# Kernel optimization log

Measured on AMD Instinct MI355X. Metric: run time of the kernel, lower is better.

The kernel has to match this reference:

```python
import jax, jax.numpy as jnp
import numpy as np

B, L, D, H = 2, 1000, 288, 8
DIM = D // H          # 36 per-head dim
DFF = 2 * D           # 576 conv-FFN hidden
KS = L // 4           # 250 sampled keys per query
NQ = L // 4           # 250 selected (active) queries
EPS = 1e-5


def _layernorm(x, g, b):
    mu = x.mean(-1, keepdims=True)
    var = ((x - mu) ** 2).mean(-1, keepdims=True)
    return (x - mu) * jax.lax.rsqrt(var + EPS) * g + b


def _prob_attention(q, k, v, index_key):
    # q,k,v: [b,h,L,dim]; index_key: [L, KS]
    b, h, l, dim = q.shape
    # sample KS keys per query row (gather): [b,h,L,KS,dim]
    k_samp = jnp.take(k, index_key, axis=2)
    # sampled scores: [b,h,L,KS]
    scores_samp = jnp.einsum('bhld,bhlkd->bhlk', q, k_samp)
    # sparsity measure M(q) = max - mean(over full l_key, as in source)
    measure = scores_samp.max(-1) - scores_samp.sum(-1) / l
    # top-NQ active queries per (b,h): [b,h,NQ]
    idx_q = jax.lax.top_k(measure, NQ)[1]
    q_sel = jnp.take_along_axis(q, idx_q[..., None], axis=2)  # [b,h,NQ,dim]
    sim = jnp.einsum('bhqd,bhkd->bhqk', q_sel, k) * (1.0 / np.sqrt(dim))
    attn = jax.nn.softmax(sim, axis=-1)
    out_sel = jnp.einsum('bhqk,bhkd->bhqd', attn, v)          # [b,h,NQ,dim]
    # lazy queries get mean(V); scatter active outputs in
    out = jnp.broadcast_to(v.mean(axis=2, keepdims=True), v.shape)
    bi = jnp.arange(b)[:, None, None]
    hi = jnp.arange(h)[None, :, None]
    out = out.at[bi, hi, idx_q].set(out_sel)
    return out  # [b,h,L,dim]


def reference(x, index_key, Wq, bq, Wk, bk, Wv, bv, W1, b1, W2, b2,
              ln1_g, ln1_b, ln2_g, ln2_b):
    b, l, d = x.shape
    # QKV projections -> [b,h,L,dim]
    q = (x @ Wq.T + bq).reshape(b, l, H, DIM).transpose(0, 2, 1, 3)
    k = (x @ Wk.T + bk).reshape(b, l, H, DIM).transpose(0, 2, 1, 3)
    v = (x @ Wv.T + bv).reshape(b, l, H, DIM).transpose(0, 2, 1, 3)
    attn = _prob_attention(q, k, v, index_key)
    attn = attn.transpose(0, 2, 1, 3).reshape(b, l, d)
    # residual + LN1 (dropout is identity in eval)
    h1 = _layernorm(x + attn, ln1_g, ln1_b)
    # conv FFN (kernel_size=1 conv == per-position linear), exact GELU
    f = jax.nn.gelu(h1 @ W1.T + b1, approximate=False)   # [b,l,DFF]
    f = jax.nn.gelu(f @ W2.T + b2, approximate=False)    # [b,l,d]
    return _layernorm(f + h1, ln2_g, ln2_b)


def setup_inputs() -> dict:
    key = jax.random.key(0)
    ks = jax.random.split(key, 10)
    s = 0.05
    return {
        'x': jax.random.normal(ks[0], (B, L, D), jnp.float32),
        'index_key': jax.random.randint(ks[1], (L, KS), 0, L),
        'Wq': jax.random.normal(ks[2], (D, D), jnp.float32) * s,
        'bq': jnp.zeros((D,), jnp.float32),
        'Wk': jax.random.normal(ks[3], (D, D), jnp.float32) * s,
        'bk': jnp.zeros((D,), jnp.float32),
        'Wv': jax.random.normal(ks[4], (D, D), jnp.float32) * s,
        'bv': jnp.zeros((D,), jnp.float32),
        'W1': jax.random.normal(ks[5], (DFF, D), jnp.float32) * s,
        'b1': jnp.zeros((DFF,), jnp.float32),
        'W2': jax.random.normal(ks[6], (D, DFF), jnp.float32) * s,
        'b2': jnp.zeros((D,), jnp.float32),
        'ln1_g': jnp.ones((D,), jnp.float32),
        'ln1_b': jnp.zeros((D,), jnp.float32),
        'ln2_g': jnp.ones((D,), jnp.float32),
        'ln2_b': jnp.zeros((D,), jnp.float32),
    }
```

## Files before the change

### kernel.cpp

```cpp
#include <hip/hip_runtime.h>
#include <math.h>

#define B_ 2
#define L_ 1000
#define D_ 288
#define H_ 8
#define DIM_ 36
#define DFF_ 576
#define KS_ 250
#define NQ_ 250
#define BH_ (B_ * H_)
#define EPS_ 1e-5f
#define PSTRIDE_ 40
#define MAXCL_ 125

__device__ __forceinline__ float gelu_exact(float x) {
    return 0.5f * x * (1.0f + erff(x * 0.70710678118654752f));
}

__device__ __forceinline__ float dot4(float4 a, float4 b) {
    return a.x * b.x + a.y * b.y + a.z * b.z + a.w * b.w;
}

__global__ __launch_bounds__(256) void weights_prep_kernel(
    const float* __restrict__ Wq, const float* __restrict__ Wk,
    const float* __restrict__ Wv,
    float* __restrict__ WqT, float* __restrict__ WkT, float* __restrict__ WvT,
    const float* __restrict__ W1, const float* __restrict__ W2,
    float* __restrict__ W1T, float* __restrict__ W2T)
{
    __shared__ float tile[32][33];
    const int tx = threadIdx.x & 31, ty = threadIdx.x >> 5;
    if (blockIdx.x < 243) {
        const int m = blockIdx.x / 81;
        const int t = blockIdx.x % 81;
        const float* src = (m == 0) ? Wq : (m == 1) ? Wk : Wv;
        float* dst = (m == 0) ? WqT : (m == 1) ? WkT : WvT;
        const int ty0 = (t / 9) * 32, tx0 = (t % 9) * 32;
#pragma unroll
        for (int i = 0; i < 4; i++)
            tile[ty + 8 * i][tx] = src[(size_t)(ty0 + ty + 8 * i) * D_ + tx0 + tx];
        __syncthreads();
#pragma unroll
        for (int i = 0; i < 4; i++)
            dst[(size_t)(tx0 + ty + 8 * i) * D_ + ty0 + tx] = tile[tx][ty + 8 * i];
    } else {
        int t = blockIdx.x - 243;
        const float* src; float* dst; int Rr, Cc, ntx;
        if (t < 162) { src = W1; dst = W1T; Rr = DFF_; Cc = D_; ntx = 9; }
        else { t -= 162; src = W2; dst = W2T; Rr = D_; Cc = DFF_; ntx = 18; }
        const int ty0 = (t / ntx) * 32, tx0 = (t % ntx) * 32;
#pragma unroll
        for (int i = 0; i < 4; i++)
            tile[ty + 8 * i][tx] = src[(size_t)(ty0 + ty + 8 * i) * Cc + tx0 + tx];
        __syncthreads();
#pragma unroll
        for (int i = 0; i < 4; i++)
            dst[(size_t)(tx0 + ty + 8 * i) * Rr + ty0 + tx] = tile[tx][ty + 8 * i];
    }
}

__global__ __launch_bounds__(448) void qkvT3_kernel(
    const float* __restrict__ x,
    const float* __restrict__ WqT, const float* __restrict__ WkT,
    const float* __restrict__ WvT,
    const float* __restrict__ bq, const float* __restrict__ bk,
    const float* __restrict__ bv,
    float* __restrict__ Q, float* __restrict__ K, float* __restrict__ V,
    float* __restrict__ KT)
{
    __shared__ float xsT[D_][4];
    __shared__ float red[3456];
    const int base = blockIdx.x * 4;
    const int tid = threadIdx.x;

    for (int idx = tid; idx < 4 * D_; idx += 448) {
        int r = idx / D_, k = idx % D_;
        xsT[k][r] = x[(size_t)(base + r) * D_ + k];
    }
    __syncthreads();

    const int kg = tid / 216;
    const int ct = tid - kg * 216;
    const bool active = tid < 432;

    float a[4][4];
    const float* WT = nullptr;
    int m = 0, c = 0;
    if (active) {
        const int gcol = 4 * ct;
        m = gcol / D_;
        c = gcol - m * D_;
        WT = (m == 0) ? WqT : (m == 1) ? WkT : WvT;
        const float* bias = (m == 0) ? bq : (m == 1) ? bk : bv;
#pragma unroll
        for (int j = 0; j < 4; j++) {
            float bv2 = (kg == 0) ? bias[c + j] : 0.f;
#pragma unroll
            for (int r = 0; r < 4; r++) a[j][r] = bv2;
        }
        const int kbeg = kg * 144;
        for (int k = kbeg; k < kbeg + 144; k++) {
            float4 w = *(const float4*)(WT + (size_t)k * D_ + c);
            float4 xv = *(const float4*)&xsT[k][0];
            a[0][0] += w.x * xv.x; a[0][1] += w.x * xv.y; a[0][2] += w.x * xv.z; a[0][3] += w.x * xv.w;
            a[1][0] += w.y * xv.x; a[1][1] += w.y * xv.y; a[1][2] += w.y * xv.z; a[1][3] += w.y * xv.w;
            a[2][0] += w.z * xv.x; a[2][1] += w.z * xv.y; a[2][2] += w.z * xv.z; a[2][3] += w.z * xv.w;
            a[3][0] += w.w * xv.x; a[3][1] += w.w * xv.y; a[3][2] += w.w * xv.z; a[3][3] += w.w * xv.w;
        }
        if (kg == 1) {
#pragma unroll
            for (int j = 0; j < 4; j++)
                *(float4*)&red[(j * 216 + ct) * 4] =
                    make_float4(a[j][0], a[j][1], a[j][2], a[j][3]);
        }
    }
    __syncthreads();

    if (active && kg == 0) {
        const int bb_ = base / L_;
        const int l0 = base % L_;
        float* outp = (m == 0) ? Q : (m == 1) ? K : V;
#pragma unroll
        for (int j = 0; j < 4; j++) {
            float4 o = *(const float4*)&red[(j * 216 + ct) * 4];
            a[j][0] += o.x; a[j][1] += o.y; a[j][2] += o.z; a[j][3] += o.w;
            int col = c + j;
            int h = col / DIM_, dd = col % DIM_;
#pragma unroll
            for (int r = 0; r < 4; r++) {
                int row = base + r;
                int b = row / L_, l = row % L_;
                outp[((size_t)(b * H_ + h) * L_ + l) * DIM_ + dd] = a[j][r];
            }
            if (m == 1) {
                *(float4*)(KT + ((size_t)(bb_ * H_ + h) * DIM_ + dd) * L_ + l0) =
                    make_float4(a[j][0], a[j][1], a[j][2], a[j][3]);
            }
        }
    }
}

__global__ __launch_bounds__(320) void qkv_kernel(
    const float* __restrict__ x,
    const float* __restrict__ Wq, const float* __restrict__ bq,
    const float* __restrict__ Wk, const float* __restrict__ bk,
    const float* __restrict__ Wv, const float* __restrict__ bv,
    float* __restrict__ Q, float* __restrict__ K, float* __restrict__ V)
{
    constexpr int R = 8;
    __shared__ float xs[R][D_];
    const int base = blockIdx.x * R;
    const int tid = threadIdx.x;

    const float4* xsrc = (const float4*)(x + (size_t)base * D_);
    float4* xdst = (float4*)&xs[0][0];
    for (int i = tid; i < R * D_ / 4; i += 320) xdst[i] = xsrc[i];
    __syncthreads();

    if (tid < D_) {
        const float4* wq4 = (const float4*)(Wq + (size_t)tid * D_);
        const float4* wk4 = (const float4*)(Wk + (size_t)tid * D_);
        const float4* wv4 = (const float4*)(Wv + (size_t)tid * D_);
        float aq[R], ak[R], av[R];
        float biasq = bq[tid], biask = bk[tid], biasv = bv[tid];
#pragma unroll
        for (int r = 0; r < R; r++) { aq[r] = biasq; ak[r] = biask; av[r] = biasv; }
        for (int d4 = 0; d4 < D_ / 4; d4++) {
            float4 wqv = wq4[d4], wkv = wk4[d4], wvv = wv4[d4];
#pragma unroll
            for (int r = 0; r < R; r++) {
                float4 hv = *(const float4*)&xs[r][d4 * 4];
                aq[r] += dot4(hv, wqv);
                ak[r] += dot4(hv, wkv);
                av[r] += dot4(hv, wvv);
            }
        }
        const int h = tid / DIM_, dd = tid % DIM_;
#pragma unroll
        for (int r = 0; r < R; r++) {
            int row = base + r;
            int b = row / L_, l = row % L_;
            size_t o = ((size_t)(b * H_ + h) * L_ + l) * DIM_ + dd;
            Q[o] = aq[r]; K[o] = ak[r]; V[o] = av[r];
        }
    }
}

__global__ __launch_bounds__(256) void score_measure3_kernel(
    const float* __restrict__ Q, const float* __restrict__ KT,
    const int* __restrict__ index_key, float* __restrict__ measure)
{
    constexpr int R = 8;
    __shared__ float qs[R][DIM_];
    __shared__ float st[R][1004];
    const int bh = blockIdx.x / 125;
    const int qt = blockIdx.x % 125;
    const int tid = threadIdx.x;

    if (tid < R * DIM_ / 4)
        ((float4*)&qs[0][0])[tid] =
            ((const float4*)(Q + ((size_t)bh * L_ + qt * R) * DIM_))[tid];
    __syncthreads();

    const float* KTb = KT + (size_t)bh * DIM_ * L_;
#pragma unroll
    for (int i = 0; i < 4; i++) {
        const int k = i * 256 + tid;
        if (k < L_) {
            float acc[R];
#pragma unroll
            for (int r = 0; r < R; r++) acc[r] = 0.f;
#pragma unroll
            for (int d4 = 0; d4 < DIM_ / 4; d4++) {
                float4 kv;
                kv.x = KTb[(size_t)(d4 * 4 + 0) * L_ + k];
                kv.y = KTb[(size_t)(d4 * 4 + 1) * L_ + k];
                kv.z = KTb[(size_t)(d4 * 4 + 2) * L_ + k];
                kv.w = KTb[(size_t)(d4 * 4 + 3) * L_ + k];
#pragma unroll
                for (int r = 0; r < R; r++)
                    acc[r] += dot4(*(const float4*)&qs[r][d4 * 4], kv);
            }
#pragma unroll
            for (int r = 0; r < R; r++) st[r][k] = acc[r];
        }
    }
    __syncthreads();

    const int r = tid >> 5;
    const int lane = tid & 31;
    const int l = qt * R + r;
    const int* ik = index_key + l * KS_;
    float mx = -1e30f, sm = 0.f;
    for (int s = lane; s < KS_; s += 32) {
        float v = st[r][ik[s]];
        mx = fmaxf(mx, v);
        sm += v;
    }
#pragma unroll
    for (int off = 16; off; off >>= 1) {
        mx = fmaxf(mx, __shfl_xor(mx, off));
        sm += __shfl_xor(sm, off);
    }
    if (lane == 0) measure[bh * L_ + l] = mx - sm * (1.0f / (float)L_);
}

__global__ __launch_bounds__(256) void measure_kernel(
    const float* __restrict__ Q, const float* __restrict__ K,
    const int* __restrict__ index_key, float* __restrict__ measure)
{
    const int w = threadIdx.x >> 6;
    const int lane = threadIdx.x & 63;
    const int wid = blockIdx.x * 4 + w;
    const int bh = wid / L_;
    const int l = wid % L_;

    const float4* qp = (const float4*)(Q + ((size_t)bh * L_ + l) * DIM_);
    float4 q[9];
#pragma unroll
    for (int i = 0; i < 9; i++) q[i] = qp[i];

    const int* ik = index_key + l * KS_;
    const float* Kb = K + (size_t)bh * L_ * DIM_;

    float mx = -1e30f, sm = 0.f;
#pragma unroll
    for (int s = lane; s < KS_; s += 64) {
        int kidx = ik[s];
        const float4* k4 = (const float4*)(Kb + (size_t)kidx * DIM_);
        float acc = 0.f;
#pragma unroll
        for (int i = 0; i < 9; i++) acc += dot4(q[i], k4[i]);
        mx = fmaxf(mx, acc);
        sm += acc;
    }
#pragma unroll
    for (int off = 32; off; off >>= 1) {
        mx = fmaxf(mx, __shfl_xor(mx, off));
        sm += __shfl_xor(sm, off);
    }
    if (lane == 0) measure[wid] = mx - sm * (1.0f / (float)L_);
}

__global__ __launch_bounds__(256) void topk_vmean_kernel(
    const float* __restrict__ measure, int* __restrict__ qlist,
    int* __restrict__ slot_map, const float* __restrict__ V,
    float* __restrict__ Vmean)
{
    if (blockIdx.x < BH_ * 4) {
        const int bh = blockIdx.x >> 2;
        const int quarter = blockIdx.x & 3;
        __shared__ float m[L_];
        for (int i = threadIdx.x; i < L_; i += 256) m[i] = measure[bh * L_ + i];
        __syncthreads();
        const int i = quarter * 250 + threadIdx.x;
        if (threadIdx.x < 250) {
            float mi = m[i];
            int rank = 0;
            for (int j = 0; j < L_; j++) {
                float mj = m[j];
                rank += (mj > mi) || (mj == mi && j < i);
            }
            if (rank < NQ_) qlist[bh * NQ_ + rank] = i;
            slot_map[bh * L_ + i] = (rank < NQ_) ? rank : -1;
        }
    } else {
        const int bh = blockIdx.x - BH_ * 4;
        const int tid = threadIdx.x;
        __shared__ float red2[7][DIM_];
        if (tid < 252) {
            int gq = tid / DIM_, d = tid % DIM_;
            const float* basep = V + (size_t)bh * L_ * DIM_;
            float s = 0.f;
            for (int l = gq; l < L_; l += 7) s += basep[l * DIM_ + d];
            red2[gq][d] = s;
        }
        __syncthreads();
        if (tid < DIM_) {
            float s = 0.f;
#pragma unroll
            for (int gq = 0; gq < 7; gq++) s += red2[gq][tid];
            Vmean[bh * DIM_ + tid] = s * (1.0f / L_);
        }
    }
}

__global__ __launch_bounds__(256) void attn_part2_kernel(
    const float* __restrict__ Q, const float* __restrict__ K,
    const float* __restrict__ V, const int* __restrict__ qlist,
    float* __restrict__ part, int nchunk, int chunk_len)
{
    __shared__ float Ks[MAXCL_ * DIM_];
    __shared__ float Vs[MAXCL_ * DIM_];
    const int bh = blockIdx.x / nchunk;
    const int chunk = blockIdx.x % nchunk;
    const int tid = threadIdx.x;
    const int k0 = chunk * chunk_len;

    {
        const float4* Ksrc = (const float4*)(K + ((size_t)bh * L_ + k0) * DIM_);
        const float4* Vsrc = (const float4*)(V + ((size_t)bh * L_ + k0) * DIM_);
        const int nf4 = chunk_len * (DIM_ / 4);
        for (int i = tid; i < nf4; i += 256) {
            ((float4*)Ks)[i] = Ksrc[i];
            ((float4*)Vs)[i] = Vsrc[i];
        }
    }
    __syncthreads();

    const int slot = tid;
    if (slot >= NQ_) return;

    const int qidx = qlist[bh * NQ_ + slot];
    const float4* qp = (const float4*)(Q + ((size_t)bh * L_ + qidx) * DIM_);
    float4 q[9];
#pragma unroll
    for (int i = 0; i < 9; i++) q[i] = qp[i];

    const float scale = (float)(1.0 / 6.0);
    float4 acc[9];
#pragma unroll
    for (int i = 0; i < 9; i++) acc[i] = make_float4(0.f, 0.f, 0.f, 0.f);
    float sum = 0.f;

    for (int j = 0; j < chunk_len; j++) {
        const float4* kp = (const float4*)(Ks + j * DIM_);
        float s = 0.f;
#pragma unroll
        for (int i = 0; i < 9; i++) s += dot4(q[i], kp[i]);
        float e = __expf(s * scale);
        sum += e;
        const float4* vp = (const float4*)(Vs + j * DIM_);
#pragma unroll
        for (int i = 0; i < 9; i++) {
            float4 vv = vp[i];
            acc[i].x += e * vv.x;
            acc[i].y += e * vv.y;
            acc[i].z += e * vv.z;
            acc[i].w += e * vv.w;
        }
    }

    float* p = part + ((size_t)(bh * NQ_ + slot) * nchunk + chunk) * PSTRIDE_;
#pragma unroll
    for (int i = 0; i < 9; i++) ((float4*)p)[i] = acc[i];
    p[DIM_] = sum;
}

__global__ __launch_bounds__(320) void combine_ln1_kernel(
    const float* __restrict__ x, const float* __restrict__ part,
    const int* __restrict__ slot_map, const float* __restrict__ Vmean,
    const float* __restrict__ g, const float* __restrict__ bb,
    float* __restrict__ h1, int nchunk)
{
    const int row = blockIdx.x;
    const int b = row / L_, l = row % L_;
    const int tid = threadIdx.x;
    __shared__ float psum[5], pssq[5];

    float y = 0.f;
    if (tid < D_) {
        const int h = tid / DIM_, d = tid % DIM_;
        const int bh = b * H_ + h;
        const int slot = slot_map[bh * L_ + l];
        float v;
        if (slot < 0) {
            v = Vmean[bh * DIM_ + d];
        } else {
            const float* p = part + (size_t)(bh * NQ_ + slot) * nchunk * PSTRIDE_;
            float a = 0.f, s = 0.f;
            for (int c = 0; c < nchunk; c++) {
                a += p[c * PSTRIDE_ + d];
                s += p[c * PSTRIDE_ + DIM_];
            }
            v = a / s;
        }
        y = x[(size_t)row * D_ + tid] + v;
    }

    float s1 = y, s2 = y * y;
#pragma unroll
    for (int off = 32; off; off >>= 1) {
        s1 += __shfl_xor(s1, off);
        s2 += __shfl_xor(s2, off);
    }
    const int w = tid >> 6, lane = tid & 63;
    if (lane == 0) { psum[w] = s1; pssq[w] = s2; }
    __syncthreads();
    float ts = 0.f, tq = 0.f;
#pragma unroll
    for (int i = 0; i < 5; i++) { ts += psum[i]; tq += pssq[i]; }
    float mu = ts * (1.0f / D_);
    float var = tq * (1.0f / D_) - mu * mu;
    float rstd = rsqrtf(var + EPS_);
    if (tid < D_)
        h1[(size_t)row * D_ + tid] = (y - mu) * rstd * g[tid] + bb[tid];
}

__global__ __launch_bounds__(576) void ffn_fused4_kernel(
    const float* __restrict__ h1,
    const float* __restrict__ W1T, const float* __restrict__ b1,
    const float* __restrict__ W2T, const float* __restrict__ b2,
    const float* __restrict__ g, const float* __restrict__ bb,
    float* __restrict__ out)
{
    constexpr int R = 4;
    __shared__ float hsT[D_][R];
    __shared__ float fsT[DFF_][R];
    __shared__ float red[8064];
    __shared__ float ys[R][D_];
    const int base = blockIdx.x * R;
    const int tid = threadIdx.x;

    for (int idx = tid; idx < R * D_; idx += 576) {
        int r = idx / D_, k = idx % D_;
        hsT[k][r] = h1[(size_t)(base + r) * D_ + k];
    }
    __syncthreads();

    {
        const int kg = tid / 144;
        const int ct = tid - kg * 144;
        const int c = 4 * ct;
        float a[4][4];
#pragma unroll
        for (int j = 0; j < 4; j++) {
            float bv = (kg == 0) ? b1[c + j] : 0.f;
#pragma unroll
            for (int r = 0; r < 4; r++) a[j][r] = bv;
        }
        const int kbeg = kg * 72;
        for (int k = kbeg; k < kbeg + 72; k++) {
            float4 w = *(const float4*)(W1T + (size_t)k * DFF_ + c);
            float4 xv = *(const float4*)&hsT[k][0];
            a[0][0] += w.x * xv.x; a[0][1] += w.x * xv.y; a[0][2] += w.x * xv.z; a[0][3] += w.x * xv.w;
            a[1][0] += w.y * xv.x; a[1][1] += w.y * xv.y; a[1][2] += w.y * xv.z; a[1][3] += w.y * xv.w;
            a[2][0] += w.z * xv.x; a[2][1] += w.z * xv.y; a[2][2] += w.z * xv.z; a[2][3] += w.z * xv.w;
            a[3][0] += w.w * xv.x; a[3][1] += w.w * xv.y; a[3][2] += w.w * xv.z; a[3][3] += w.w * xv.w;
        }
        if (kg >= 1) {
#pragma unroll
            for (int j = 0; j < 4; j++)
                *(float4*)&red[(((kg - 1) * 576) + j * 144 + ct) * 4] =
                    make_float4(a[j][0], a[j][1], a[j][2], a[j][3]);
        }
        __syncthreads();
        if (kg == 0) {
#pragma unroll
            for (int j = 0; j < 4; j++) {
                float4 o0 = *(const float4*)&red[((0 * 576) + j * 144 + ct) * 4];
                float4 o1 = *(const float4*)&red[((1 * 576) + j * 144 + ct) * 4];
                float4 o2 = *(const float4*)&red[((2 * 576) + j * 144 + ct) * 4];
                float y0 = gelu_exact(a[j][0] + o0.x + o1.x + o2.x);
                float y1 = gelu_exact(a[j][1] + o0.y + o1.y + o2.y);
                float y2 = gelu_exact(a[j][2] + o0.z + o1.z + o2.z);
                float y3 = gelu_exact(a[j][3] + o0.w + o1.w + o2.w);
                *(float4*)&fsT[c + j][0] = make_float4(y0, y1, y2, y3);
            }
        }
    }
    __syncthreads();

    {
        const int kg = tid / 72;
        const int ct = tid - kg * 72;
        const int c = 4 * ct;
        float a[4][4];
#pragma unroll
        for (int j = 0; j < 4; j++) {
            float bv = (kg == 0) ? b2[c + j] : 0.f;
#pragma unroll
            for (int r = 0; r < 4; r++) a[j][r] = bv;
        }
        const int kbeg = kg * 72;
        for (int k = kbeg; k < kbeg + 72; k++) {
            float4 w = *(const float4*)(W2T + (size_t)k * D_ + c);
            float4 fv = *(const float4*)&fsT[k][0];
            a[0][0] += w.x * fv.x; a[0][1] += w.x * fv.y; a[0][2] += w.x * fv.z; a[0][3] += w.x * fv.w;
            a[1][0] += w.y * fv.x; a[1][1] += w.y * fv.y; a[1][2] += w.y * fv.z; a[1][3] += w.y * fv.w;
            a[2][0] += w.z * fv.x; a[2][1] += w.z * fv.y; a[2][2] += w.z * fv.z; a[2][3] += w.z * fv.w;
            a[3][0] += w.w * fv.x; a[3][1] += w.w * fv.y; a[3][2] += w.w * fv.z; a[3][3] += w.w * fv.w;
        }
        if (kg >= 1) {
#pragma unroll
            for (int j = 0; j < 4; j++)
                *(float4*)&red[(((kg - 1) * 288) + j * 72 + ct) * 4] =
                    make_float4(a[j][0], a[j][1], a[j][2], a[j][3]);
        }
        __syncthreads();
        if (kg == 0) {
            float y[4][4];
#pragma unroll
            for (int j = 0; j < 4; j++) {
                float t0 = a[j][0], t1 = a[j][1], t2 = a[j][2], t3 = a[j][3];
#pragma unroll
                for (int kk = 0; kk < 7; kk++) {
                    float4 o = *(const float4*)&red[((kk * 288) + j * 72 + ct) * 4];
                    t0 += o.x; t1 += o.y; t2 += o.z; t3 += o.w;
                }
                float4 hres = *(const float4*)&hsT[c + j][0];
                y[j][0] = gelu_exact(t0) + hres.x;
                y[j][1] = gelu_exact(t1) + hres.y;
                y[j][2] = gelu_exact(t2) + hres.z;
                y[j][3] = gelu_exact(t3) + hres.w;
            }
#pragma unroll
            for (int r = 0; r < 4; r++)
                *(float4*)&ys[r][c] = make_float4(y[0][r], y[1][r], y[2][r], y[3][r]);
        }
    }
    __syncthreads();

    const int w = tid >> 6;
    const int lane = tid & 63;
    if (w < 4) {
        const int r = w;
        float s = 0.f, ss = 0.f;
#pragma unroll
        for (int i = 0; i < 5; i++) {
            int j = lane + i * 64;
            if (j < D_) { float yv = ys[r][j]; s += yv; ss += yv * yv; }
        }
#pragma unroll
        for (int off = 32; off; off >>= 1) {
            s += __shfl_xor(s, off);
            ss += __shfl_xor(ss, off);
        }
        float mu = s * (1.0f / D_);
        float var = ss * (1.0f / D_) - mu * mu;
        float rstd = rsqrtf(var + EPS_);
        int row = base + r;
#pragma unroll
        for (int i = 0; i < 5; i++) {
            int j = lane + i * 64;
            if (j < D_)
                out[(size_t)row * D_ + j] = (ys[r][j] - mu) * rstd * g[j] + bb[j];
        }
    }
}

__global__ __launch_bounds__(192) void ffn1_kernel(
    const float* __restrict__ h1,
    const float* __restrict__ W1, const float* __restrict__ b1,
    float* __restrict__ f1)
{
    constexpr int R = 8;
    __shared__ float hs[R][D_];
    const int base = blockIdx.x * R;
    const int tid = threadIdx.x;

    const float4* hsrc = (const float4*)(h1 + (size_t)base * D_);
    float4* hdst = (float4*)&hs[0][0];
    for (int i = tid; i < R * D_ / 4; i += 192) hdst[i] = hsrc[i];
    __syncthreads();

    const int j0 = tid, j1 = tid + 192, j2 = tid + 384;
    const float4* w0 = (const float4*)(W1 + (size_t)j0 * D_);
    const float4* w1 = (const float4*)(W1 + (size_t)j1 * D_);
    const float4* w2 = (const float4*)(W1 + (size_t)j2 * D_);
    float a0[R], a1[R], a2[R];
    float bb0 = b1[j0], bb1 = b1[j1], bb2 = b1[j2];
#pragma unroll
    for (int r = 0; r < R; r++) { a0[r] = bb0; a1[r] = bb1; a2[r] = bb2; }

    for (int d4 = 0; d4 < D_ / 4; d4++) {
        float4 x0 = w0[d4], x1 = w1[d4], x2 = w2[d4];
#pragma unroll
        for (int r = 0; r < R; r++) {
            float4 hv = *(const float4*)&hs[r][d4 * 4];
            a0[r] += dot4(hv, x0);
            a1[r] += dot4(hv, x1);
            a2[r] += dot4(hv, x2);
        }
    }
#pragma unroll
    for (int r = 0; r < R; r++) {
        size_t rowo = (size_t)(base + r) * DFF_;
        f1[rowo + j0] = gelu_exact(a0[r]);
        f1[rowo + j1] = gelu_exact(a1[r]);
        f1[rowo + j2] = gelu_exact(a2[r]);
    }
}

__global__ __launch_bounds__(320) void ffn2_ln_kernel(
    const float* __restrict__ f1, const float* __restrict__ h1,
    const float* __restrict__ W2, const float* __restrict__ b2,
    const float* __restrict__ g, const float* __restrict__ bb,
    float* __restrict__ out)
{
    constexpr int R = 8;
    __shared__ float fs[R][DFF_];
    __shared__ float hs[R][D_];
    __shared__ float ys[R][D_];
    const int base = blockIdx.x * R;
    const int tid = threadIdx.x;

    const float4* fsrc = (const float4*)(f1 + (size_t)base * DFF_);
    float4* fdst = (float4*)&fs[0][0];
    for (int i = tid; i < R * DFF_ / 4; i += 320) fdst[i] = fsrc[i];
    const float4* hsrc = (const float4*)(h1 + (size_t)base * D_);
    float4* hdst = (float4*)&hs[0][0];
    for (int i = tid; i < R * D_ / 4; i += 320) hdst[i] = hsrc[i];
    __syncthreads();

    if (tid < D_) {
        const float4* w4 = (const float4*)(W2 + (size_t)tid * DFF_);
        float acc[R];
        float bias = b2[tid];
#pragma unroll
        for (int r = 0; r < R; r++) acc[r] = bias;
        for (int d4 = 0; d4 < DFF_ / 4; d4++) {
            float4 wv = w4[d4];
#pragma unroll
            for (int r = 0; r < R; r++) {
                float4 fv = *(const float4*)&fs[r][d4 * 4];
                acc[r] += dot4(fv, wv);
            }
        }
#pragma unroll
        for (int r = 0; r < R; r++) ys[r][tid] = gelu_exact(acc[r]) + hs[r][tid];
    }
    __syncthreads();

    const int w = tid >> 6;
    const int lane = tid & 63;
    for (int r = w; r < R; r += 5) {
        float s = 0.f, ss = 0.f;
#pragma unroll
        for (int i = 0; i < 5; i++) {
            int j = lane + i * 64;
            if (j < D_) { float y = ys[r][j]; s += y; ss += y * y; }
        }
#pragma unroll
        for (int off = 32; off; off >>= 1) {
            s += __shfl_xor(s, off);
            ss += __shfl_xor(ss, off);
        }
        float mu = s * (1.0f / D_);
        float var = ss * (1.0f / D_) - mu * mu;
        float rstd = rsqrtf(var + EPS_);
        int row = base + r;
#pragma unroll
        for (int i = 0; i < 5; i++) {
            int j = lane + i * 64;
            if (j < D_) out[(size_t)row * D_ + j] = (ys[r][j] - mu) * rstd * g[j] + bb[j];
        }
    }
}

extern "C" void kernel_launch(void* const* d_in, const int* in_sizes, int n_in,
                              void* d_out, int out_size, void* d_ws, size_t ws_size,
                              hipStream_t stream)
{
    const float* x         = (const float*)d_in[0];
    const int*   index_key = (const int*)  d_in[1];
    const float* Wq = (const float*)d_in[2];
    const float* bq = (const float*)d_in[3];
    const float* Wk = (const float*)d_in[4];
    const float* bk = (const float*)d_in[5];
    const float* Wv = (const float*)d_in[6];
    const float* bv = (const float*)d_in[7];
    const float* W1 = (const float*)d_in[8];
    const float* b1 = (const float*)d_in[9];
    const float* W2 = (const float*)d_in[10];
    const float* b2 = (const float*)d_in[11];
    const float* ln1_g = (const float*)d_in[12];
    const float* ln1_b = (const float*)d_in[13];
    const float* ln2_g = (const float*)d_in[14];
    const float* ln2_b = (const float*)d_in[15];
    float* out = (float*)d_out;

    float* Q        = (float*)d_ws;
    float* K        = Q + 576000;
    float* V        = K + 576000;
    float* Vmean    = V + 576000;
    float* measure  = Vmean + 576;
    float* wtbuf    = measure + 16000;
    float* h1       = wtbuf + 576000;
    int*   qlist    = (int*)(h1 + 576000);
    int*   slot_map = qlist + 4000;
    float* part     = (float*)(slot_map + 16000);
    float* f1       = part;
    float* KT       = part + 4000000;

    float* WqT = part;
    float* WkT = WqT + 82944;
    float* WvT = WkT + 82944;
    float* W1T = wtbuf;
    float* W2T = wtbuf + 165888;

    const size_t kt_end = 2916576ull + 4000000ull + 576000ull;
    const bool   big    = ws_size >= kt_end * sizeof(float);
    const int    nchunk = big ? 25 : 8;
    const int    chunk_len = L_ / nchunk;

    if (big) {
        weights_prep_kernel<<<567, 256, 0, stream>>>(Wq, Wk, Wv, WqT, WkT, WvT,
                                                     W1, W2, W1T, W2T);
        qkvT3_kernel<<<500, 448, 0, stream>>>(x, WqT, WkT, WvT, bq, bk, bv,
                                              Q, K, V, KT);
        score_measure3_kernel<<<BH_ * 125, 256, 0, stream>>>(Q, KT, index_key, measure);
    } else {
        qkv_kernel<<<250, 320, 0, stream>>>(x, Wq, bq, Wk, bk, Wv, bv, Q, K, V);
        measure_kernel<<<4000, 256, 0, stream>>>(Q, K, index_key, measure);
    }
    topk_vmean_kernel<<<BH_ * 4 + BH_, 256, 0, stream>>>(measure, qlist, slot_map, V, Vmean);
    attn_part2_kernel<<<BH_ * nchunk, 256, 0, stream>>>(Q, K, V, qlist, part, nchunk, chunk_len);
    combine_ln1_kernel<<<B_ * L_, 320, 0, stream>>>(x, part, slot_map, Vmean,
                                                    ln1_g, ln1_b, h1, nchunk);
    if (big) {
        ffn_fused4_kernel<<<500, 576, 0, stream>>>(h1, W1T, b1, W2T, b2,
                                                   ln2_g, ln2_b, out);
    } else {
        ffn1_kernel<<<250, 192, 0, stream>>>(h1, W1, b1, f1);
        ffn2_ln_kernel<<<250, 320, 0, stream>>>(f1, h1, W2, b2, ln2_g, ln2_b, out);
    }
}
```

Baseline: 253.8 us.

## Split fused FFN into tiled GEMM1 and GEMM2+LayerNorm kernels

Replaces the single fused FFN kernel, which handled 4 rows per block and re-read the full W1T/W2T from global memory for every block, with two kernels. The first computes h1·W1T+b1 with GELU over 32-row by 64-column tiles and writes f1 to global memory. The second computes the W2 product, GELU, residual and LayerNorm over 8 rows per block using a 2-way K split. Larger row tiles cut redundant weight traffic, at the cost of an extra launch and a round-trip of the f1 intermediate through global memory.

Result: slower. 273.5 us (+7.8%).

```diff
diff --git a/kernel.cpp b/kernel.cpp
--- a/kernel.cpp
+++ b/kernel.cpp
@@ -85,13 +85,12 @@
     const bool active = tid < 432;
 
     float a[4][4];
-    const float* WT = nullptr;
     int m = 0, c = 0;
     if (active) {
         const int gcol = 4 * ct;
         m = gcol / D_;
         c = gcol - m * D_;
-        WT = (m == 0) ? WqT : (m == 1) ? WkT : WvT;
+        const float* WT = (m == 0) ? WqT : (m == 1) ? WkT : WvT;
         const float* bias = (m == 0) ? bq : (m == 1) ? bk : bv;
 #pragma unroll
         for (int j = 0; j < 4; j++) {
@@ -438,123 +437,136 @@
         h1[(size_t)row * D_ + tid] = (y - mu) * rstd * g[tid] + bb[tid];
 }
 
-__global__ __launch_bounds__(576) void ffn_fused4_kernel(
-    const float* __restrict__ h1,
-    const float* __restrict__ W1T, const float* __restrict__ b1,
+__global__ __launch_bounds__(256) void ffn_gemm1_kernel(
+    const float* __restrict__ h1, const float* __restrict__ W1T,
+    const float* __restrict__ b1, float* __restrict__ f1)
+{
+    __shared__ float hsT[D_][34];
+    const int bx = blockIdx.x / 9;
+    const int tile_c = (blockIdx.x % 9) * 64;
+    const int base = bx * 32;
+    const int tid = threadIdx.x;
+
+    for (int idx = tid; idx < 32 * 72; idx += 256) {
+        int row = idx / 72, k4 = idx % 72;
+        int gr = base + row; if (gr > B_ * L_ - 1) gr = B_ * L_ - 1;
+        float4 v = *(const float4*)(h1 + (size_t)gr * D_ + 4 * k4);
+        hsT[4 * k4 + 0][row] = v.x;
+        hsT[4 * k4 + 1][row] = v.y;
+        hsT[4 * k4 + 2][row] = v.z;
+        hsT[4 * k4 + 3][row] = v.w;
+    }
+    __syncthreads();
+
+    const int cg = tid & 15, rg = tid >> 4;
+    const int c = tile_c + 4 * cg;
+    const int r0 = 2 * rg;
+
+    float4 bias = *(const float4*)(b1 + c);
+    float a00 = bias.x, a01 = bias.y, a02 = bias.z, a03 = bias.w;
+    float a10 = bias.x, a11 = bias.y, a12 = bias.z, a13 = bias.w;
+
+    const float* wp = W1T + c;
+    for (int k = 0; k < D_; k++) {
+        float4 w = *(const float4*)wp; wp += DFF_;
+        float x0 = hsT[k][r0], x1 = hsT[k][r0 + 1];
+        a00 += w.x * x0; a01 += w.y * x0; a02 += w.z * x0; a03 += w.w * x0;
+        a10 += w.x * x1; a11 += w.y * x1; a12 += w.z * x1; a13 += w.w * x1;
+    }
+
+    int row0 = base + r0;
+    if (row0 < B_ * L_) {
+        float4 y0 = make_float4(gelu_exact(a00), gelu_exact(a01),
+                                gelu_exact(a02), gelu_exact(a03));
+        *(float4*)(f1 + (size_t)row0 * DFF_ + c) = y0;
+    }
+    if (row0 + 1 < B_ * L_) {
+        float4 y1 = make_float4(gelu_exact(a10), gelu_exact(a11),
+                                gelu_exact(a12), gelu_exact(a13));
+        *(float4*)(f1 + (size_t)(row0 + 1) * DFF_ + c) = y1;
+    }
+}
+
+__global__ __launch_bounds__(576) void ffn_gemm2_kernel(
+    const float* __restrict__ f1, const float* __restrict__ h1,
     const float* __restrict__ W2T, const float* __restrict__ b2,
     const float* __restrict__ g, const float* __restrict__ bb,
     float* __restrict__ out)
 {
-    constexpr int R = 4;
-    __shared__ float hsT[D_][R];
-    __shared__ float fsT[DFF_][R];
-    __shared__ float red[8064];
-    __shared__ float ys[R][D_];
-    const int base = blockIdx.x * R;
-    const int tid = threadIdx.x;
-
-    for (int idx = tid; idx < R * D_; idx += 576) {
-        int r = idx / D_, k = idx % D_;
-        hsT[k][r] = h1[(size_t)(base + r) * D_ + k];
-    }
-    __syncthreads();
-
+    __shared__ float fsT[DFF_][10];
+    __shared__ float hs[8][D_];
+    __shared__ float red[8 * D_];
+    __shared__ float ys[8][D_];
+    const int base = blockIdx.x * 8;
+    const int tid = threadIdx.x;
+
+    for (int idx = tid; idx < 8 * 144; idx += 576) {
+        int row = idx / 144, k4 = idx % 144;
+        float4 v = *(const float4*)(f1 + (size_t)(base + row) * DFF_ + 4 * k4);
+        fsT[4 * k4 + 0][row] = v.x;
+        fsT[4 * k4 + 1][row] = v.y;
+        fsT[4 * k4 + 2][row] = v.z;
+        fsT[4 * k4 + 3][row] = v.w;
+    }
     {
-        const int kg = tid / 144;
-        const int ct = tid - kg * 144;
-        const int c = 4 * ct;
-        float a[4][4];
-#pragma unroll
-        for (int j = 0; j < 4; j++) {
-            float bv = (kg == 0) ? b1[c + j] : 0.f;
-#pragma unroll
-            for (int r = 0; r < 4; r++) a[j][r] = bv;
-        }
-        const int kbeg = kg * 72;
-        for (int k = kbeg; k < kbeg + 72; k++) {
-            float4 w = *(const float4*)(W1T + (size_t)k * DFF_ + c);
-            float4 xv = *(const float4*)&hsT[k][0];
-            a[0][0] += w.x * xv.x; a[0][1] += w.x * xv.y; a[0][2] += w.x * xv.z; a[0][3] += w.x * xv.w;
-            a[1][0] += w.y * xv.x; a[1][1] += w.y * xv.y; a[1][2] += w.y * xv.z; a[1][3] += w.y * xv.w;
-            a[2][0] += w.z * xv.x; a[2][1] += w.z * xv.y; a[2][2] += w.z * xv.z; a[2][3] += w.z * xv.w;
-            a[3][0] += w.w * xv.x; a[3][1] += w.w * xv.y; a[3][2] += w.w * xv.z; a[3][3] += w.w * xv.w;
-        }
-        if (kg >= 1) {
-#pragma unroll
-            for (int j = 0; j < 4; j++)
-                *(float4*)&red[(((kg - 1) * 576) + j * 144 + ct) * 4] =
-                    make_float4(a[j][0], a[j][1], a[j][2], a[j][3]);
-        }
-        __syncthreads();
-        if (kg == 0) {
-#pragma unroll
-            for (int j = 0; j < 4; j++) {
-                float4 o0 = *(const float4*)&red[((0 * 576) + j * 144 + ct) * 4];
-                float4 o1 = *(const float4*)&red[((1 * 576) + j * 144 + ct) * 4];
-                float4 o2 = *(const float4*)&red[((2 * 576) + j * 144 + ct) * 4];
-                float y0 = gelu_exact(a[j][0] + o0.x + o1.x + o2.x);
-                float y1 = gelu_exact(a[j][1] + o0.y + o1.y + o2.y);
-                float y2 = gelu_exact(a[j][2] + o0.z + o1.z + o2.z);
-                float y3 = gelu_exact(a[j][3] + o0.w + o1.w + o2.w);
-                *(float4*)&fsT[c + j][0] = make_float4(y0, y1, y2, y3);
-            }
-        }
-    }
-    __syncthreads();
-
-    {
-        const int kg = tid / 72;
-        const int ct = tid - kg * 72;
-        const int c = 4 * ct;
-        float a[4][4];
-#pragma unroll
-        for (int j = 0; j < 4; j++) {
-            float bv = (kg == 0) ? b2[c + j] : 0.f;
-#pragma unroll
-            for (int r = 0; r < 4; r++) a[j][r] = bv;
-        }
-        const int kbeg = kg * 72;
-        for (int k = kbeg; k < kbeg + 72; k++) {
-            float4 w = *(const float4*)(W2T + (size_t)k * D_ + c);
-            float4 fv = *(const float4*)&fsT[k][0];
-            a[0][0] += w.x * fv.x; a[0][1] += w.x * fv.y; a[0][2] += w.x * fv.z; a[0][3] += w.x * fv.w;
-            a[1][0] += w.y * fv.x; a[1][1] += w.y * fv.y; a[1][2] += w.y * fv.z; a[1][3] += w.y * fv.w;
-            a[2][0] += w.z * fv.x; a[2][1] += w.z * fv.y; a[2][2] += w.z * fv.z; a[2][3] += w.z * fv.w;
-            a[3][0] += w.w * fv.x; a[3][1] += w.w * fv.y; a[3][2] += w.w * fv.z; a[3][3] += w.w * fv.w;
-        }
-        if (kg >= 1) {
-#pragma unroll
-            for (int j = 0; j < 4; j++)
-                *(float4*)&red[(((kg - 1) * 288) + j * 72 + ct) * 4] =
-                    make_float4(a[j][0], a[j][1], a[j][2], a[j][3]);
-        }
-        __syncthreads();
-        if (kg == 0) {
-            float y[4][4];
-#pragma unroll
-            for (int j = 0; j < 4; j++) {
-                float t0 = a[j][0], t1 = a[j][1], t2 = a[j][2], t3 = a[j][3];
-#pragma unroll
-                for (int kk = 0; kk < 7; kk++) {
-                    float4 o = *(const float4*)&red[((kk * 288) + j * 72 + ct) * 4];
-                    t0 += o.x; t1 += o.y; t2 += o.z; t3 += o.w;
-                }
-                float4 hres = *(const float4*)&hsT[c + j][0];
-                y[j][0] = gelu_exact(t0) + hres.x;
-                y[j][1] = gelu_exact(t1) + hres.y;
-                y[j][2] = gelu_exact(t2) + hres.z;
-                y[j][3] = gelu_exact(t3) + hres.w;
-            }
-#pragma unroll
-            for (int r = 0; r < 4; r++)
-                *(float4*)&ys[r][c] = make_float4(y[0][r], y[1][r], y[2][r], y[3][r]);
-        }
+        int row = tid / 72, k4 = tid % 72;
+        ((float4*)&hs[row][0])[k4] =
+            *(const float4*)(h1 + (size_t)(base + row) * D_ + 4 * k4);
+    }
+    __syncthreads();
+
+    const int kg = tid / 288;
+    const int t2 = tid - kg * 288;
+    const int rg = t2 / 72;
+    const int cg = t2 - rg * 72;
+    const int c = 4 * cg;
+    const int r0 = 2 * rg;
+
+    float a00, a01, a02, a03, a10, a11, a12, a13;
+    if (kg == 0) {
+        float4 bias = *(const float4*)(b2 + c);
+        a00 = bias.x; a01 = bias.y; a02 = bias.z; a03 = bias.w;
+        a10 = bias.x; a11 = bias.y; a12 = bias.z; a13 = bias.w;
+    } else {
+        a00 = a01 = a02 = a03 = a10 = a11 = a12 = a13 = 0.f;
+    }
+
+    const int kbeg = kg * 288;
+    const float* wp = W2T + (size_t)kbeg * D_ + c;
+    for (int kk = 0; kk < 288; kk++) {
+        float4 w = *(const float4*)wp; wp += D_;
+        int k = kbeg + kk;
+        float x0 = fsT[k][r0], x1 = fsT[k][r0 + 1];
+        a00 += w.x * x0; a01 += w.y * x0; a02 += w.z * x0; a03 += w.w * x0;
+        a10 += w.x * x1; a11 += w.y * x1; a12 += w.z * x1; a13 += w.w * x1;
+    }
+
+    if (kg == 1) {
+        *(float4*)&red[r0 * D_ + c] = make_float4(a00, a01, a02, a03);
+        *(float4*)&red[(r0 + 1) * D_ + c] = make_float4(a10, a11, a12, a13);
+    }
+    __syncthreads();
+    if (kg == 0) {
+        float4 o0 = *(const float4*)&red[r0 * D_ + c];
+        float4 o1 = *(const float4*)&red[(r0 + 1) * D_ + c];
+        float4 h0 = *(const float4*)&hs[r0][c];
+        float4 h1v = *(const float4*)&hs[r0 + 1][c];
+        float4 y0 = make_float4(gelu_exact(a00 + o0.x) + h0.x,
+                                gelu_exact(a01 + o0.y) + h0.y,
+                                gelu_exact(a02 + o0.z) + h0.z,
+                                gelu_exact(a03 + o0.w) + h0.w);
+        float4 y1 = make_float4(gelu_exact(a10 + o1.x) + h1v.x,
+                                gelu_exact(a11 + o1.y) + h1v.y,
+                                gelu_exact(a12 + o1.z) + h1v.z,
+                                gelu_exact(a13 + o1.w) + h1v.w);
+        *(float4*)&ys[r0][c] = y0;
+        *(float4*)&ys[r0 + 1][c] = y1;
     }
     __syncthreads();
 
     const int w = tid >> 6;
     const int lane = tid & 63;
-    if (w < 4) {
+    if (w < 8) {
         const int r = w;
         float s = 0.f, ss = 0.f;
 #pragma unroll
@@ -750,8 +762,9 @@
     combine_ln1_kernel<<<B_ * L_, 320, 0, stream>>>(x, part, slot_map, Vmean,
                                                     ln1_g, ln1_b, h1, nchunk);
     if (big) {
-        ffn_fused4_kernel<<<500, 576, 0, stream>>>(h1, W1T, b1, W2T, b2,
-                                                   ln2_g, ln2_b, out);
+        ffn_gemm1_kernel<<<567, 256, 0, stream>>>(h1, W1T, b1, f1);
+        ffn_gemm2_kernel<<<250, 576, 0, stream>>>(f1, h1, W2T, b2,
+                                                  ln2_g, ln2_b, out);
     } else {
         ffn1_kernel<<<250, 192, 0, stream>>>(h1, W1, b1, f1);
         ffn2_ln_kernel<<<250, 320, 0, stream>>>(f1, h1, W2, b2, ln2_g, ln2_b, out);
```
